# Kernel optimization log

Measured on AMD Instinct MI355X. Metric: run time of the kernel, lower is better.

Reference implementation:

```python
import jax, jax.numpy as jnp
import numpy as np

N = 50000      # nodes
E = 800000     # edges
P = 200000     # link pairs
D_IN = 128     # input_dim
F_NUM = 128    # filter_num
OUT = 2        # out_dim
K = 10         # APPNP propagation steps
ALPHA = 0.1    # teleport prob


def setup_inputs() -> dict:
    key = jax.random.key(0)
    ks = jax.random.split(key, 9)
    x = jax.random.normal(ks[0], (N, D_IN), dtype=jnp.float32)
    edge_index = jax.random.randint(ks[1], (2, E), 0, N)
    index = jax.random.randint(ks[2], (P, 2), 0, N)
    s1 = 1.0 / np.sqrt(D_IN)
    s2 = 1.0 / np.sqrt(F_NUM)
    s3 = 1.0 / np.sqrt(2 * F_NUM)
    W1 = jax.random.uniform(ks[3], (F_NUM, D_IN), minval=-s1, maxval=s1)
    b1 = jax.random.uniform(ks[4], (F_NUM,), minval=-s1, maxval=s1)
    W2 = jax.random.uniform(ks[5], (F_NUM, F_NUM), minval=-s2, maxval=s2)
    b2 = jax.random.uniform(ks[6], (F_NUM,), minval=-s2, maxval=s2)
    W3 = jax.random.uniform(ks[7], (OUT, 2 * F_NUM), minval=-s3, maxval=s3)
    b3 = jax.random.uniform(ks[8], (OUT,), minval=-s3, maxval=s3)
    return {"x": x, "edge_index": edge_index, "index": index,
            "W1": W1, "b1": b1, "W2": W2, "b2": b2, "W3": W3, "b3": b3}


def _gcn_norm(edge_index, num_nodes):
    # PyG gcn_norm: add self-loops, sym norm D^{-1/2} (A+I) D^{-1/2}
    src, dst = edge_index[0], edge_index[1]
    loop = jnp.arange(num_nodes, dtype=src.dtype)
    src = jnp.concatenate([src, loop])
    dst = jnp.concatenate([dst, loop])
    deg = jax.ops.segment_sum(jnp.ones_like(src, dtype=jnp.float32), dst,
                              num_segments=num_nodes)
    dinv = jnp.where(deg > 0, jax.lax.rsqrt(deg), 0.0)
    norm = dinv[src] * dinv[dst]  # [E+N]
    return src, dst, norm


def _appnp(x, src, dst, norm, num_nodes):
    # h_{k+1} = (1-alpha) * A_hat h_k + alpha * x0
    def step(h, _):
        agg = jax.ops.segment_sum(norm[:, None] * h[src], dst,
                                  num_segments=num_nodes)
        return (1.0 - ALPHA) * agg + ALPHA * x, None
    h, _ = jax.lax.scan(step, x, None, length=K)
    return h


def reference(x, edge_index, index, W1, b1, W2, b2, W3, b3):
    num_nodes = x.shape[0]
    src, dst, norm = _gcn_norm(edge_index, num_nodes)
    h = x @ W1.T + b1                      # [N, F]
    h = jax.nn.relu(_appnp(h, src, dst, norm, num_nodes))
    h = h @ W2.T + b2                      # [N, F]
    h = jax.nn.relu(_appnp(h, src, dst, norm, num_nodes))
    feat = jnp.concatenate([h[index[:, 0]], h[index[:, 1]]], axis=-1)  # [P, 2F]
    out = feat @ W3.T + b3                 # [P, OUT]
    return jax.nn.log_softmax(out, axis=1)
```

## Files before the change

### kernel.cpp

```cpp
#include <hip/hip_runtime.h>
#include <math.h>

#define NN 50000
#define NE 800000
#define NP 200000
#define NF 128
#define NEDGE_TOT (NE + NN)
#define NBLK 196
#define NBK 64
#define DPB 782
#define BKCAP 16384
#define EPB 2048

typedef __attribute__((ext_vector_type(8))) short short8;
typedef __attribute__((ext_vector_type(4))) float float4v;
typedef __attribute__((ext_vector_type(2))) _Float16 h2;

__device__ __forceinline__ float bf_lo(unsigned u) { return __uint_as_float(u << 16); }
__device__ __forceinline__ float bf_hi(unsigned u) { return __uint_as_float(u & 0xffff0000u); }
__device__ __forceinline__ unsigned short f2bf(float f) {
    unsigned u = __float_as_uint(f);
    return (unsigned short)((u + 0x7fffu + ((u >> 16) & 1u)) >> 16);
}
__device__ __forceinline__ unsigned pack2bf(float a, float b) {
    return (unsigned)f2bf(a) | ((unsigned)f2bf(b) << 16);
}

__device__ __forceinline__ h2 u2h2(unsigned u) {
    union { unsigned u; h2 h; } c; c.u = u; return c.h;
}
__device__ __forceinline__ unsigned h22u(h2 h) {
    union { unsigned u; h2 h; } c; c.h = h; return c.u;
}
__device__ __forceinline__ float h_lo(unsigned u) { return (float)u2h2(u).x; }
__device__ __forceinline__ float h_hi(unsigned u) { return (float)u2h2(u).y; }
__device__ __forceinline__ unsigned pack2h(float a, float b) {
    h2 h; h.x = (_Float16)a; h.y = (_Float16)b; return h22u(h);
}

__global__ __launch_bounds__(256) void init_cnt_k(int* __restrict__ cnt) {
    int i = blockIdx.x * 256 + threadIdx.x;
    if (i < NN) cnt[i] = 1;
}

__global__ __launch_bounds__(256) void count_k(const int* __restrict__ ei,
                                               int* __restrict__ cnt) {
    int e = blockIdx.x * 256 + threadIdx.x;
    if (e < NE) atomicAdd(&cnt[ei[NE + e]], 1);
}

__global__ __launch_bounds__(256) void scan_reduce_k(const int* __restrict__ cnt,
                                                     int* __restrict__ bsum,
                                                     float* __restrict__ dinv) {
    __shared__ int s[256];
    int t = threadIdx.x;
    int idx = blockIdx.x * 256 + t;
    int v = (idx < NN) ? cnt[idx] : 0;
    if (idx < NN) dinv[idx] = rsqrtf((float)v);
    s[t] = v;
    __syncthreads();
    for (int off = 128; off > 0; off >>= 1) {
        if (t < off) s[t] += s[t + off];
        __syncthreads();
    }
    if (t == 0) bsum[blockIdx.x] = s[0];
}

__global__ __launch_bounds__(256) void scan_bsums_k(const int* __restrict__ bsum,
                                                    int* __restrict__ boff) {
    __shared__ int s[256];
    int t = threadIdx.x;
    int v = (t < NBLK) ? bsum[t] : 0;
    s[t] = v;
    __syncthreads();
    for (int off = 1; off < 256; off <<= 1) {
        int add = (t >= off) ? s[t - off] : 0;
        __syncthreads();
        s[t] += add;
        __syncthreads();
    }
    if (t < NBLK) boff[t] = s[t] - v;
}

__global__ __launch_bounds__(256) void scan_down_k(const int* __restrict__ cnt,
                                                   const int* __restrict__ boff,
                                                   int* __restrict__ row_ptr) {
    __shared__ int s[256];
    int t = threadIdx.x;
    int idx = blockIdx.x * 256 + t;
    int v = (idx < NN) ? cnt[idx] : 0;
    s[t] = v;
    __syncthreads();
    for (int off = 1; off < 256; off <<= 1) {
        int add = (t >= off) ? s[t - off] : 0;
        __syncthreads();
        s[t] += add;
        __syncthreads();
    }
    int excl = s[t] - v + boff[blockIdx.x];
    if (idx < NN) {
        row_ptr[idx] = excl;
        if (idx == NN - 1) row_ptr[NN] = excl + v;
    }
}

__global__ __launch_bounds__(256) void bin_k(const int* __restrict__ ei,
                                             int* __restrict__ gtail,
                                             int2* __restrict__ gbk) {
    __shared__ int cntA[NBK], baseA[NBK], gposA[NBK];
    __shared__ int2 stage[EPB];
    int tid = threadIdx.x;
    int ebase = blockIdx.x * EPB;
    int sv[8], dv[8], lp8[8], bk8[8];
    bool val[8];
    if (tid < NBK) cntA[tid] = 0;
    __syncthreads();
#pragma unroll
    for (int k = 0; k < 8; ++k) {
        int e = ebase + k * 256 + tid;
        val[k] = (e < NEDGE_TOT);
        if (val[k]) {
            int s, d;
            if (e < NE) { s = ei[e]; d = ei[NE + e]; }
            else        { s = d = e - NE; }
            sv[k] = s; dv[k] = d;
            bk8[k] = d / DPB;
            lp8[k] = atomicAdd(&cntA[bk8[k]], 1);
        }
    }
    __syncthreads();
    if (tid == 0) {
        int run = 0;
        for (int b = 0; b < NBK; ++b) { baseA[b] = run; run += cntA[b]; }
    }
    __syncthreads();
    if (tid < NBK && cntA[tid] > 0)
        gposA[tid] = atomicAdd(&gtail[tid], cntA[tid]);
    __syncthreads();
#pragma unroll
    for (int k = 0; k < 8; ++k)
        if (val[k]) {
            int2 r; r.x = sv[k]; r.y = dv[k];
            stage[baseA[bk8[k]] + lp8[k]] = r;
        }
    __syncthreads();
    int total = baseA[NBK - 1] + cntA[NBK - 1];
    for (int i = tid; i < total; i += 256) {
        int2 r = stage[i];
        int b = r.y / DPB;
        gbk[(size_t)b * BKCAP + gposA[b] + (i - baseA[b])] = r;
    }
}

__global__ __launch_bounds__(256) void build_k(const int* __restrict__ row_ptr,
                                               const int* __restrict__ gtail,
                                               const int2* __restrict__ gbk,
                                               int* __restrict__ cols) {
    __shared__ int wcur[DPB];
    int tid = threadIdx.x;
    int b = blockIdx.x;
    int d0 = b * DPB;
    for (int i = tid; i < DPB; i += 256) {
        int d = d0 + i;
        wcur[i] = (d < NN) ? row_ptr[d] : 0;
    }
    __syncthreads();
    int nb = gtail[b];
    const int2* src = gbk + (size_t)b * BKCAP;
    for (int t = tid; t < nb; t += 256) {
        int2 r = src[t];
        int pos = atomicAdd(&wcur[r.y - d0], 1);
        cols[pos] = r.x;
    }
}

__global__ __launch_bounds__(256) void zero_k(unsigned short* Ys1, unsigned short* Ys2,
                                              unsigned short* HA, unsigned short* HB,
                                              int* gtail) {
    int t = threadIdx.x;
    unsigned short* bufs[4] = {Ys1, Ys2, HA, HB};
    unsigned short* b = bufs[t >> 6];
    ((unsigned*)(b + (size_t)NN * NF))[t & 63] = 0u;
    if (t < NBK) gtail[t] = 0;
}

__global__ __launch_bounds__(256) void cast_w_k(const float* __restrict__ W,
                                                unsigned short* __restrict__ Wb) {
    int t = blockIdx.x * 256 + threadIdx.x;
    if (t >= 128 * 128 / 8) return;
    int i = t * 8;
    float4 f0 = *(const float4*)(W + i);
    float4 f1 = *(const float4*)(W + i + 4);
    uint4 q;
    q.x = pack2bf(f0.x, f0.y);
    q.y = pack2bf(f0.z, f0.w);
    q.z = pack2bf(f1.x, f1.y);
    q.w = pack2bf(f1.z, f1.w);
    *(uint4*)(Wb + i) = q;
}

#define GPAD 136
template <bool F32IN>
__global__ __launch_bounds__(256) void gemm_mfma_k(const void* __restrict__ Xv,
                                                   const unsigned short* __restrict__ Wb,
                                                   const float* __restrict__ bias,
                                                   const float* __restrict__ dinv,
                                                   unsigned short* __restrict__ Yu,
                                                   unsigned short* __restrict__ Ys,
                                                   int nrows) {
    __shared__ unsigned short sm[4 * 16 * GPAD];
    int wave = threadIdx.x >> 6, lane = threadIdx.x & 63;
    int rbase = blockIdx.x * 64 + wave * 16;
    if (rbase >= nrows) return;
    int quad = lane >> 4, mn = lane & 15;
    float4v acc[8];
#pragma unroll
    for (int ft = 0; ft < 8; ++ft) acc[ft] = (float4v){0.f, 0.f, 0.f, 0.f};
#pragma unroll
    for (int kb = 0; kb < 128; kb += 32) {
        short8 a;
        if (F32IN) {
            const float* X = (const float*)Xv;
            float4 f0 = *(const float4*)(X + (size_t)(rbase + mn) * NF + kb + quad * 8);
            float4 f1 = *(const float4*)(X + (size_t)(rbase + mn) * NF + kb + quad * 8 + 4);
            a[0] = (short)f2bf(f0.x); a[1] = (short)f2bf(f0.y);
            a[2] = (short)f2bf(f0.z); a[3] = (short)f2bf(f0.w);
            a[4] = (short)f2bf(f1.x); a[5] = (short)f2bf(f1.y);
            a[6] = (short)f2bf(f1.z); a[7] = (short)f2bf(f1.w);
        } else {
            const unsigned short* X = (const unsigned short*)Xv;
            a = *(const short8*)(X + (size_t)(rbase + mn) * NF + kb + quad * 8);
        }
#pragma unroll
        for (int ft = 0; ft < 8; ++ft) {
            short8 b = *(const short8*)(Wb + (size_t)(ft * 16 + mn) * NF + kb + quad * 8);
            acc[ft] = __builtin_amdgcn_mfma_f32_16x16x32_bf16(a, b, acc[ft], 0, 0, 0);
        }
    }
    unsigned short* smw = sm + wave * 16 * GPAD;
#pragma unroll
    for (int ft = 0; ft < 8; ++ft) {
        float bv = bias[ft * 16 + mn];
#pragma unroll
        for (int r = 0; r < 4; ++r) {
            union { _Float16 h; unsigned short s; } cv;
            cv.h = (_Float16)(acc[ft][r] + bv);
            smw[(quad * 4 + r) * GPAD + ft * 16 + mn] = cv.s;
        }
    }
    __syncthreads();
#pragma unroll
    for (int t = 0; t < 4; ++t) {
        int rl = t * 4 + quad;
        int row = rbase + rl;
        uint4 q = *(const uint4*)(smw + rl * GPAD + mn * 8);
        *(uint4*)(Yu + (size_t)row * NF + mn * 8) = q;
        float g = dinv[row];
        uint4 qs;
        qs.x = pack2h(g * h_lo(q.x), g * h_hi(q.x));
        qs.y = pack2h(g * h_lo(q.y), g * h_hi(q.y));
        qs.z = pack2h(g * h_lo(q.z), g * h_hi(q.z));
        qs.w = pack2h(g * h_lo(q.w), g * h_hi(q.w));
        *(uint4*)(Ys + (size_t)row * NF + mn * 8) = qs;
    }
}

__global__ __launch_bounds__(256) void appnp_h_k(const unsigned short* __restrict__ hs,
                                                 const unsigned short* __restrict__ x0,
                                                 const float* __restrict__ dinv,
                                                 unsigned short* __restrict__ out,
                                                 const int* __restrict__ row_ptr,
                                                 const int* __restrict__ cols,
                                                 int mode,
                                                 const float* __restrict__ W3,
                                                 float4* __restrict__ puv) {
    int wid = (blockIdx.x * 256 + threadIdx.x) >> 6;
    int lane = threadIdx.x & 63;
    if (wid >= NN) return;
    int half = lane >> 5, li = lane & 31;
    int beg = row_ptr[wid], end = row_ptr[wid + 1];
    uint2 xq = make_uint2(0u, 0u);
    if (half == 0) xq = *((const uint2*)(x0 + (size_t)wid * NF) + li);
    h2 a01; a01.x = (_Float16)0.f; a01.y = (_Float16)0.f;
    h2 a23 = a01;
    for (int e = beg; e < end; e += 64) {
        int m = end - e;
        if (m > 64) m = 64;
        int c = (lane < m) ? cols[e + lane] : NN;
        for (int j = 0; j < m; j += 16) {
            uint2 q[8];
#pragma unroll
            for (int p = 0; p < 8; ++p) {
                int cj = __shfl(c, j + 2 * p + half, 64);
                q[p] = *((const uint2*)(hs + (size_t)cj * NF) + li);
            }
#pragma unroll
            for (int p = 0; p < 8; ++p) {
                a01 += u2h2(q[p].x);
                a23 += u2h2(q[p].y);
            }
        }
    }
    a01 += u2h2((unsigned)__shfl_xor((int)h22u(a01), 32, 64));
    a23 += u2h2((unsigned)__shfl_xor((int)h22u(a23), 32, 64));
    if (half != 0) return;
    float g = dinv[wid];
    float s9 = 0.9f * g;
    float h0 = s9 * (float)a01.x + 0.1f * h_lo(xq.x);
    float h1 = s9 * (float)a01.y + 0.1f * h_hi(xq.x);
    float h2v = s9 * (float)a23.x + 0.1f * h_lo(xq.y);
    float h3 = s9 * (float)a23.y + 0.1f * h_hi(xq.y);
    if (mode == 0) {
        uint2 oq;
        oq.x = pack2h(g * h0, g * h1);
        oq.y = pack2h(g * h2v, g * h3);
        *((uint2*)(out + (size_t)wid * NF) + li) = oq;
    } else {
        h0 = fmaxf(h0, 0.f); h1 = fmaxf(h1, 0.f);
        h2v = fmaxf(h2v, 0.f); h3 = fmaxf(h3, 0.f);
        if (mode == 1) {
            uint2 oq;
            oq.x = pack2bf(h0, h1);
            oq.y = pack2bf(h2v, h3);
            *((uint2*)(out + (size_t)wid * NF) + li) = oq;
        } else {
            int fb = li * 4;
            float4 wu0 = *(const float4*)(W3 + fb);
            float4 wv0 = *(const float4*)(W3 + 128 + fb);
            float4 wu1 = *(const float4*)(W3 + 256 + fb);
            float4 wv1 = *(const float4*)(W3 + 384 + fb);
            float du0 = h0 * wu0.x + h1 * wu0.y + h2v * wu0.z + h3 * wu0.w;
            float du1 = h0 * wu1.x + h1 * wu1.y + h2v * wu1.z + h3 * wu1.w;
            float dv0 = h0 * wv0.x + h1 * wv0.y + h2v * wv0.z + h3 * wv0.w;
            float dv1 = h0 * wv1.x + h1 * wv1.y + h2v * wv1.z + h3 * wv1.w;
#pragma unroll
            for (int off = 1; off < 32; off <<= 1) {
                du0 += __shfl_xor(du0, off, 64);
                du1 += __shfl_xor(du1, off, 64);
                dv0 += __shfl_xor(dv0, off, 64);
                dv1 += __shfl_xor(dv1, off, 64);
            }
            if (li == 0) puv[wid] = make_float4(du0, du1, dv0, dv1);
        }
    }
}

__global__ __launch_bounds__(256) void pair2_k(const float4* __restrict__ puv,
                                               const int2* __restrict__ index,
                                               const float* __restrict__ b3,
                                               float* __restrict__ outp) {
    int p = blockIdx.x * 256 + threadIdx.x;
    if (p >= NP) return;
    int2 uv = index[p];
    float4 a = puv[uv.x];
    float4 b = puv[uv.y];
    float s0 = a.x + b.z + b3[0];
    float s1 = a.y + b.w + b3[1];
    float m = fmaxf(s0, s1);
    float lse = m + logf(expf(s0 - m) + expf(s1 - m));
    *(float2*)(outp + (size_t)p * 2) = make_float2(s0 - lse, s1 - lse);
}

extern "C" void kernel_launch(void* const* d_in, const int* in_sizes, int n_in,
                              void* d_out, int out_size, void* d_ws, size_t ws_size,
                              hipStream_t stream) {
    const float* x  = (const float*)d_in[0];
    const int* ei   = (const int*)d_in[1];
    const int* idx  = (const int*)d_in[2];
    const float* W1 = (const float*)d_in[3];
    const float* b1 = (const float*)d_in[4];
    const float* W2 = (const float*)d_in[5];
    const float* b2 = (const float*)d_in[6];
    const float* W3 = (const float*)d_in[7];
    const float* b3 = (const float*)d_in[8];
    float* out = (float*)d_out;

    char* ws = (char*)d_ws;
    size_t off = 0;
    auto alloc = [&](size_t bytes) -> void* {
        void* p = ws + off;
        off = (off + bytes + 255) & ~(size_t)255;
        return p;
    };
    const size_t HROWS = (size_t)(NN + 1) * NF;
    int*   cnt     = (int*)  alloc(NN * sizeof(int));
    float* dinv    = (float*)alloc(NN * sizeof(float));
    int*   row_ptr = (int*)  alloc((NN + 1) * sizeof(int));
    int*   bsum    = (int*)  alloc(NBLK * sizeof(int));
    int*   boff    = (int*)  alloc(NBLK * sizeof(int));
    int*   gtail   = (int*)  alloc(NBK * sizeof(int));
    int2*  gbk     = (int2*) alloc((size_t)NBK * BKCAP * sizeof(int2));
    int*   cols    = (int*)  alloc((size_t)NEDGE_TOT * sizeof(int));
    float4* puv    = (float4*)alloc((size_t)NN * sizeof(float4));
    unsigned short* Wb1 = (unsigned short*)alloc(128 * 128 * 2);
    unsigned short* Wb2 = (unsigned short*)alloc(128 * 128 * 2);
    unsigned short* Yu1 = (unsigned short*)alloc(HROWS * 2);
    unsigned short* Ys1 = (unsigned short*)alloc(HROWS * 2);
    unsigned short* Yu2 = (unsigned short*)alloc(HROWS * 2);
    unsigned short* Ys2 = (unsigned short*)alloc(HROWS * 2);
    unsigned short* HA  = (unsigned short*)alloc(HROWS * 2);
    unsigned short* HB  = (unsigned short*)alloc(HROWS * 2);
    unsigned short* Hrelu = (unsigned short*)alloc((size_t)NN * NF * 2);

    const int gN    = (NN + 255) / 256;
    const int gE    = (NE + 255) / 256;
    const int gBin  = (NEDGE_TOT + EPB - 1) / EPB;
    const int gGemm = (NN + 63) / 64;
    const int gStep = (NN * 64 + 255) / 256;
    const int gPair = (NP + 255) / 256;

    cast_w_k<<<8, 256, 0, stream>>>(W1, Wb1);
    cast_w_k<<<8, 256, 0, stream>>>(W2, Wb2);
    zero_k<<<1, 256, 0, stream>>>(Ys1, Ys2, HA, HB, gtail);
    init_cnt_k<<<gN, 256, 0, stream>>>(cnt);
    count_k<<<gE, 256, 0, stream>>>(ei, cnt);
    scan_reduce_k<<<NBLK, 256, 0, stream>>>(cnt, bsum, dinv);
    scan_bsums_k<<<1, 256, 0, stream>>>(bsum, boff);
    scan_down_k<<<NBLK, 256, 0, stream>>>(cnt, boff, row_ptr);
    bin_k<<<gBin, 256, 0, stream>>>(ei, gtail, gbk);
    build_k<<<NBK, 256, 0, stream>>>(row_ptr, gtail, gbk, cols);

    gemm_mfma_k<true><<<gGemm, 256, 0, stream>>>(x, Wb1, b1, dinv, Yu1, Ys1, NN);
    {
        const unsigned short* cur = Ys1;
        for (int k = 0; k < 10; ++k) {
            unsigned short* dst = (k == 9) ? Hrelu : ((k & 1) ? HB : HA);
            appnp_h_k<<<gStep, 256, 0, stream>>>(cur, Yu1, dinv, dst, row_ptr,
                                                 cols, (k == 9) ? 1 : 0, W3, puv);
            cur = dst;
        }
    }
    gemm_mfma_k<false><<<gGemm, 256, 0, stream>>>(Hrelu, Wb2, b2, dinv, Yu2, Ys2, NN);
    {
        const unsigned short* cur = Ys2;
        for (int k = 0; k < 10; ++k) {
            unsigned short* dst = (k & 1) ? HB : HA;
            appnp_h_k<<<gStep, 256, 0, stream>>>(cur, Yu2, dinv, dst, row_ptr,
                                                 cols, (k == 9) ? 2 : 0, W3, puv);
            cur = dst;
        }
    }
    pair2_k<<<gPair, 256, 0, stream>>>(puv, (const int2*)idx, b3, out);
}
```

Baseline: 835.7 us.

## Split feature matrices into 32-column chunks for cache-local APPNP propagation

Stores every hidden-feature buffer as four column-chunk planes of 32 features and rewrites the propagation kernel so each 16-lane group handles one node within a single chunk. Blocks are interleaved so neighbouring blocks cover the same node range across chunks. This shrinks the gathered working set per pass (one 64-byte chunk per neighbour) so it fits L2/MALL better. The cost is re-reading CSR indices four times per step and writing partial per-chunk dot products that the pair kernel must now sum.

New measurement: 855.7 us. +2.4%, slower.

```diff
diff --git a/kernel.cpp b/kernel.cpp
--- a/kernel.cpp
+++ b/kernel.cpp
@@ -11,6 +11,9 @@
 #define DPB 782
 #define BKCAP 16384
 #define EPB 2048
+#define CROWS ((size_t)(NN + 1) * 32)
+#define NODEBLK 3128
+#define GSTEPC (8 * ((NODEBLK + 1) / 2))
 
 typedef __attribute__((ext_vector_type(8))) short short8;
 typedef __attribute__((ext_vector_type(4))) float float4v;
@@ -180,7 +183,8 @@
     int t = threadIdx.x;
     unsigned short* bufs[4] = {Ys1, Ys2, HA, HB};
     unsigned short* b = bufs[t >> 6];
-    ((unsigned*)(b + (size_t)NN * NF))[t & 63] = 0u;
+    int chunk = (t >> 4) & 3;
+    ((unsigned*)(b + (size_t)chunk * CROWS + (size_t)NN * 32))[t & 15] = 0u;
     if (t < NBK) gtail[t] = 0;
 }
 
@@ -229,7 +233,8 @@
             a[6] = (short)f2bf(f1.z); a[7] = (short)f2bf(f1.w);
         } else {
             const unsigned short* X = (const unsigned short*)Xv;
-            a = *(const short8*)(X + (size_t)(rbase + mn) * NF + kb + quad * 8);
+            a = *(const short8*)(X + (size_t)(kb >> 5) * CROWS +
+                                (size_t)(rbase + mn) * 32 + quad * 8);
         }
 #pragma unroll
         for (int ft = 0; ft < 8; ++ft) {
@@ -254,108 +259,100 @@
         int rl = t * 4 + quad;
         int row = rbase + rl;
         uint4 q = *(const uint4*)(smw + rl * GPAD + mn * 8);
-        *(uint4*)(Yu + (size_t)row * NF + mn * 8) = q;
+        size_t dst = (size_t)(mn >> 2) * CROWS + (size_t)row * 32 + (mn & 3) * 8;
+        *(uint4*)(Yu + dst) = q;
         float g = dinv[row];
         uint4 qs;
         qs.x = pack2h(g * h_lo(q.x), g * h_hi(q.x));
         qs.y = pack2h(g * h_lo(q.y), g * h_hi(q.y));
         qs.z = pack2h(g * h_lo(q.z), g * h_hi(q.z));
         qs.w = pack2h(g * h_lo(q.w), g * h_hi(q.w));
-        *(uint4*)(Ys + (size_t)row * NF + mn * 8) = qs;
-    }
-}
-
-__global__ __launch_bounds__(256) void appnp_h_k(const unsigned short* __restrict__ hs,
-                                                 const unsigned short* __restrict__ x0,
-                                                 const float* __restrict__ dinv,
-                                                 unsigned short* __restrict__ out,
-                                                 const int* __restrict__ row_ptr,
-                                                 const int* __restrict__ cols,
-                                                 int mode,
-                                                 const float* __restrict__ W3,
-                                                 float4* __restrict__ puv) {
-    int wid = (blockIdx.x * 256 + threadIdx.x) >> 6;
-    int lane = threadIdx.x & 63;
-    if (wid >= NN) return;
-    int half = lane >> 5, li = lane & 31;
-    int beg = row_ptr[wid], end = row_ptr[wid + 1];
-    uint2 xq = make_uint2(0u, 0u);
-    if (half == 0) xq = *((const uint2*)(x0 + (size_t)wid * NF) + li);
-    h2 a01; a01.x = (_Float16)0.f; a01.y = (_Float16)0.f;
-    h2 a23 = a01;
-    for (int e = beg; e < end; e += 64) {
+        *(uint4*)(Ys + dst) = qs;
+    }
+}
+
+__global__ __launch_bounds__(256) void appnp_c2_k(const unsigned short* __restrict__ hs,
+                                                  const unsigned short* __restrict__ x0c,
+                                                  const float* __restrict__ dinv,
+                                                  unsigned short* __restrict__ out,
+                                                  const int* __restrict__ row_ptr,
+                                                  const int* __restrict__ cols,
+                                                  int mode,
+                                                  const float* __restrict__ W3,
+                                                  float4* __restrict__ puvP) {
+    int bid8 = blockIdx.x & 7;
+    int chunk = bid8 >> 1;
+    int nodeBlk = (blockIdx.x >> 3) * 2 + (bid8 & 1);
+    int grp = threadIdx.x >> 4;
+    int li = threadIdx.x & 15;
+    int node = nodeBlk * 16 + grp;
+    if (node >= NN) return;
+    int gb = (threadIdx.x & 63) & ~15;
+    const unsigned short* hc = hs + (size_t)chunk * CROWS;
+    int beg = row_ptr[node], end = row_ptr[node + 1];
+    h2 acc; acc.x = (_Float16)0.f; acc.y = (_Float16)0.f;
+    for (int e = beg; e < end; e += 16) {
         int m = end - e;
-        if (m > 64) m = 64;
-        int c = (lane < m) ? cols[e + lane] : NN;
-        for (int j = 0; j < m; j += 16) {
-            uint2 q[8];
-#pragma unroll
-            for (int p = 0; p < 8; ++p) {
-                int cj = __shfl(c, j + 2 * p + half, 64);
-                q[p] = *((const uint2*)(hs + (size_t)cj * NF) + li);
-            }
-#pragma unroll
-            for (int p = 0; p < 8; ++p) {
-                a01 += u2h2(q[p].x);
-                a23 += u2h2(q[p].y);
-            }
-        }
-    }
-    a01 += u2h2((unsigned)__shfl_xor((int)h22u(a01), 32, 64));
-    a23 += u2h2((unsigned)__shfl_xor((int)h22u(a23), 32, 64));
-    if (half != 0) return;
-    float g = dinv[wid];
+        if (m > 16) m = 16;
+        int c = (li < m) ? cols[e + li] : NN;
+        for (int j = 0; j < m; j += 4) {
+            int c0 = __shfl(c, gb + j, 64);
+            int c1 = __shfl(c, gb + j + 1, 64);
+            int c2 = __shfl(c, gb + j + 2, 64);
+            int c3 = __shfl(c, gb + j + 3, 64);
+            unsigned q0 = *(const unsigned*)(hc + (size_t)c0 * 32 + li * 2);
+            unsigned q1 = *(const unsigned*)(hc + (size_t)c1 * 32 + li * 2);
+            unsigned q2 = *(const unsigned*)(hc + (size_t)c2 * 32 + li * 2);
+            unsigned q3 = *(const unsigned*)(hc + (size_t)c3 * 32 + li * 2);
+            acc += (u2h2(q0) + u2h2(q1)) + (u2h2(q2) + u2h2(q3));
+        }
+    }
+    float g = dinv[node];
     float s9 = 0.9f * g;
-    float h0 = s9 * (float)a01.x + 0.1f * h_lo(xq.x);
-    float h1 = s9 * (float)a01.y + 0.1f * h_hi(xq.x);
-    float h2v = s9 * (float)a23.x + 0.1f * h_lo(xq.y);
-    float h3 = s9 * (float)a23.y + 0.1f * h_hi(xq.y);
+    unsigned xq = *(const unsigned*)(x0c + (size_t)chunk * CROWS + (size_t)node * 32 + li * 2);
+    float h0 = s9 * (float)acc.x + 0.1f * h_lo(xq);
+    float h1 = s9 * (float)acc.y + 0.1f * h_hi(xq);
+    size_t oidx = (size_t)chunk * CROWS + (size_t)node * 32 + li * 2;
     if (mode == 0) {
-        uint2 oq;
-        oq.x = pack2h(g * h0, g * h1);
-        oq.y = pack2h(g * h2v, g * h3);
-        *((uint2*)(out + (size_t)wid * NF) + li) = oq;
+        *(unsigned*)(out + oidx) = pack2h(g * h0, g * h1);
     } else {
-        h0 = fmaxf(h0, 0.f); h1 = fmaxf(h1, 0.f);
-        h2v = fmaxf(h2v, 0.f); h3 = fmaxf(h3, 0.f);
+        h0 = fmaxf(h0, 0.f);
+        h1 = fmaxf(h1, 0.f);
         if (mode == 1) {
-            uint2 oq;
-            oq.x = pack2bf(h0, h1);
-            oq.y = pack2bf(h2v, h3);
-            *((uint2*)(out + (size_t)wid * NF) + li) = oq;
+            *(unsigned*)(out + oidx) = pack2bf(h0, h1);
         } else {
-            int fb = li * 4;
-            float4 wu0 = *(const float4*)(W3 + fb);
-            float4 wv0 = *(const float4*)(W3 + 128 + fb);
-            float4 wu1 = *(const float4*)(W3 + 256 + fb);
-            float4 wv1 = *(const float4*)(W3 + 384 + fb);
-            float du0 = h0 * wu0.x + h1 * wu0.y + h2v * wu0.z + h3 * wu0.w;
-            float du1 = h0 * wu1.x + h1 * wu1.y + h2v * wu1.z + h3 * wu1.w;
-            float dv0 = h0 * wv0.x + h1 * wv0.y + h2v * wv0.z + h3 * wv0.w;
-            float dv1 = h0 * wv1.x + h1 * wv1.y + h2v * wv1.z + h3 * wv1.w;
-#pragma unroll
-            for (int off = 1; off < 32; off <<= 1) {
+            int f = chunk * 32 + li * 2;
+            float du0 = h0 * W3[f] + h1 * W3[f + 1];
+            float du1 = h0 * W3[256 + f] + h1 * W3[256 + f + 1];
+            float dv0 = h0 * W3[128 + f] + h1 * W3[128 + f + 1];
+            float dv1 = h0 * W3[384 + f] + h1 * W3[384 + f + 1];
+#pragma unroll
+            for (int off = 1; off < 16; off <<= 1) {
                 du0 += __shfl_xor(du0, off, 64);
                 du1 += __shfl_xor(du1, off, 64);
                 dv0 += __shfl_xor(dv0, off, 64);
                 dv1 += __shfl_xor(dv1, off, 64);
             }
-            if (li == 0) puv[wid] = make_float4(du0, du1, dv0, dv1);
-        }
-    }
-}
-
-__global__ __launch_bounds__(256) void pair2_k(const float4* __restrict__ puv,
+            if (li == 0) puvP[(size_t)node * 4 + chunk] = make_float4(du0, du1, dv0, dv1);
+        }
+    }
+}
+
+__global__ __launch_bounds__(256) void pair2_k(const float4* __restrict__ puvP,
                                                const int2* __restrict__ index,
                                                const float* __restrict__ b3,
                                                float* __restrict__ outp) {
     int p = blockIdx.x * 256 + threadIdx.x;
     if (p >= NP) return;
     int2 uv = index[p];
-    float4 a = puv[uv.x];
-    float4 b = puv[uv.y];
-    float s0 = a.x + b.z + b3[0];
-    float s1 = a.y + b.w + b3[1];
+    float s0 = b3[0], s1 = b3[1];
+#pragma unroll
+    for (int c = 0; c < 4; ++c) {
+        float4 a = puvP[(size_t)uv.x * 4 + c];
+        float4 b = puvP[(size_t)uv.y * 4 + c];
+        s0 += a.x + b.z;
+        s1 += a.y + b.w;
+    }
     float m = fmaxf(s0, s1);
     float lse = m + logf(expf(s0 - m) + expf(s1 - m));
     *(float2*)(outp + (size_t)p * 2) = make_float2(s0 - lse, s1 - lse);
@@ -382,7 +379,7 @@
         off = (off + bytes + 255) & ~(size_t)255;
         return p;
     };
-    const size_t HROWS = (size_t)(NN + 1) * NF;
+    const size_t HBYTES = 4 * CROWS * 2;
     int*   cnt     = (int*)  alloc(NN * sizeof(int));
     float* dinv    = (float*)alloc(NN * sizeof(float));
     int*   row_ptr = (int*)  alloc((NN + 1) * sizeof(int));
@@ -391,22 +388,21 @@
     int*   gtail   = (int*)  alloc(NBK * sizeof(int));
     int2*  gbk     = (int2*) alloc((size_t)NBK * BKCAP * sizeof(int2));
     int*   cols    = (int*)  alloc((size_t)NEDGE_TOT * sizeof(int));
-    float4* puv    = (float4*)alloc((size_t)NN * sizeof(float4));
+    float4* puvP   = (float4*)alloc((size_t)NN * 4 * sizeof(float4));
     unsigned short* Wb1 = (unsigned short*)alloc(128 * 128 * 2);
     unsigned short* Wb2 = (unsigned short*)alloc(128 * 128 * 2);
-    unsigned short* Yu1 = (unsigned short*)alloc(HROWS * 2);
-    unsigned short* Ys1 = (unsigned short*)alloc(HROWS * 2);
-    unsigned short* Yu2 = (unsigned short*)alloc(HROWS * 2);
-    unsigned short* Ys2 = (unsigned short*)alloc(HROWS * 2);
-    unsigned short* HA  = (unsigned short*)alloc(HROWS * 2);
-    unsigned short* HB  = (unsigned short*)alloc(HROWS * 2);
-    unsigned short* Hrelu = (unsigned short*)alloc((size_t)NN * NF * 2);
+    unsigned short* Yu1 = (unsigned short*)alloc(HBYTES);
+    unsigned short* Ys1 = (unsigned short*)alloc(HBYTES);
+    unsigned short* Yu2 = (unsigned short*)alloc(HBYTES);
+    unsigned short* Ys2 = (unsigned short*)alloc(HBYTES);
+    unsigned short* HA  = (unsigned short*)alloc(HBYTES);
+    unsigned short* HB  = (unsigned short*)alloc(HBYTES);
+    unsigned short* Hrelu = (unsigned short*)alloc(HBYTES);
 
     const int gN    = (NN + 255) / 256;
     const int gE    = (NE + 255) / 256;
     const int gBin  = (NEDGE_TOT + EPB - 1) / EPB;
     const int gGemm = (NN + 63) / 64;
-    const int gStep = (NN * 64 + 255) / 256;
     const int gPair = (NP + 255) / 256;
 
     cast_w_k<<<8, 256, 0, stream>>>(W1, Wb1);
@@ -425,8 +421,8 @@
         const unsigned short* cur = Ys1;
         for (int k = 0; k < 10; ++k) {
             unsigned short* dst = (k == 9) ? Hrelu : ((k & 1) ? HB : HA);
-            appnp_h_k<<<gStep, 256, 0, stream>>>(cur, Yu1, dinv, dst, row_ptr,
-                                                 cols, (k == 9) ? 1 : 0, W3, puv);
+            appnp_c2_k<<<GSTEPC, 256, 0, stream>>>(cur, Yu1, dinv, dst, row_ptr,
+                                                   cols, (k == 9) ? 1 : 0, W3, puvP);
             cur = dst;
         }
     }
@@ -435,10 +431,10 @@
         const unsigned short* cur = Ys2;
         for (int k = 0; k < 10; ++k) {
             unsigned short* dst = (k & 1) ? HB : HA;
-            appnp_h_k<<<gStep, 256, 0, stream>>>(cur, Yu2, dinv, dst, row_ptr,
-                                                 cols, (k == 9) ? 2 : 0, W3, puv);
+            appnp_c2_k<<<GSTEPC, 256, 0, stream>>>(cur, Yu2, dinv, dst, row_ptr,
+                                                   cols, (k == 9) ? 2 : 0, W3, puvP);
             cur = dst;
         }
     }
-    pair2_k<<<gPair, 256, 0, stream>>>(puv, (const int2*)idx, b3, out);
-}
+    pair2_k<<<gPair, 256, 0, stream>>>(puvP, (const int2*)idx, b3, out);
+}
```
